# Performance work log

Hardware: AMD Instinct MI355X
Metric: run time of the kernel (lower is better)

## Reference

```python
import jax, jax.numpy as jnp
import numpy as np

EPS = 1e-07

def setup_inputs() -> dict:
    key = jax.random.key(0)
    kx, kw, kb, ku = jax.random.split(key, 4)
    B, S, D, A = 1024, 512, 200, 100
    x = jax.random.normal(kx, (B, S, D), dtype=jnp.float32)
    W = jax.random.normal(kw, (D, A), dtype=jnp.float32)
    b = jax.random.normal(kb, (A,), dtype=jnp.float32)
    u = jax.random.normal(ku, (A, 1), dtype=jnp.float32)
    return {"x": x, "W": W, "b": b, "u": u}

def reference(x, W, b, u):
    # uit: [B,S,A] = tanh(x @ W + b)
    uit = jnp.tanh(jnp.einsum('bsd,da->bsa', x, W) + b)
    # ait: [B,S] raw scores -> exp -> normalize over seq (faithful: no max-subtract)
    ait = jnp.exp(jnp.einsum('bsa,a->bs', uit, u[:, 0]))
    ait = ait / (jnp.sum(ait, axis=1, keepdims=True) + EPS)
    # weighted sum pool over seq: [B,D]
    return jnp.einsum('bsd,bs->bd', x, ait)
```

## Files before the change

### kernel.cpp

```cpp
#include <hip/hip_runtime.h>
#include <math.h>


typedef _Float16 half8 __attribute__((ext_vector_type(8)));
typedef float float4_ __attribute__((ext_vector_type(4)));

#define B_   1024
#define S_   512
#define D_   200
#define A_   100
#define NPAD 128
#define KPAD 224
#define SC   64
#define PITCH 228

#define WT_BYTES (NPAD * KPAD * 2)

__global__ void prep_kernel(const float* __restrict__ W,
                            const float* __restrict__ bias,
                            const float* __restrict__ u,
                            void* __restrict__ ws) {
  _Float16* wt = (_Float16*)ws;
  float* upad = (float*)((char*)ws + WT_BYTES);
  float* bpad = upad + NPAD;
  int idx = blockIdx.x * 256 + threadIdx.x;
  if (idx < NPAD * KPAD) {
    int n = idx / KPAD;
    int k = idx % KPAD;
    float v = (n < A_ && k < D_) ? W[k * A_ + n] : 0.f;
    wt[idx] = (_Float16)v;
  }
  if (blockIdx.x == 0 && threadIdx.x < NPAD) {
    int t = threadIdx.x;
    upad[t] = (t < A_) ? u[t] : 0.f;
    bpad[t] = (t < A_) ? bias[t] : 0.f;
  }
}

__global__ __launch_bounds__(256, 2)
void attn_kernel(const float* __restrict__ x,
                 const void* __restrict__ ws,
                 float* __restrict__ out) {
  __shared__ float xs[SC * PITCH];
  __shared__ float score_part[4][SC];
  __shared__ float e_lds[SC];

  const int b    = blockIdx.x;
  const int tid  = threadIdx.x;
  const int lane = tid & 63;
  const int wave = tid >> 6;
  const int lm   = lane & 15;
  const int lq   = lane >> 4;

  const _Float16* wt = (const _Float16*)ws;
  const float* upad = (const float*)((const char*)ws + WT_BYTES);
  const float* bpad = upad + NPAD;

  half8 Bfrag[2][7];
  float ureg[2], breg[2];
#pragma unroll
  for (int nn = 0; nn < 2; ++nn) {
    int a = (2 * wave + nn) * 16 + lm;
#pragma unroll
    for (int k = 0; k < 7; ++k) {
      Bfrag[nn][k] = *(const half8*)(wt + (size_t)a * KPAD + k * 32 + lq * 8);
    }
    ureg[nn] = upad[a];
    breg[nn] = bpad[a];
  }

  float acc_out = 0.f, den = 0.f;

  for (int chunk = 0; chunk < S_ / SC; ++chunk) {
    __syncthreads();

    {
      int c  = tid & 63;
      int r0 = tid >> 6;
      const float* xg = x + ((size_t)b * S_ + (size_t)chunk * SC) * D_;
#pragma unroll
      for (int j = 0; j < 16; ++j) {
        int row = r0 + 4 * j;
        if (c < 50) {
          float4_ v = *(const float4_*)(xg + row * D_ + c * 4);
          *(float4_*)(&xs[row * PITCH + c * 4]) = v;
        } else if (c < 57) {
          float4_ z = {0.f, 0.f, 0.f, 0.f};
          *(float4_*)(&xs[row * PITCH + c * 4]) = z;
        }
      }
    }
    __syncthreads();

    float4_ acc[4][2];
#pragma unroll
    for (int m = 0; m < 4; ++m)
#pragma unroll
      for (int nn = 0; nn < 2; ++nn)
        acc[m][nn] = (float4_){0.f, 0.f, 0.f, 0.f};

#pragma unroll
    for (int k = 0; k < 7; ++k) {
      half8 af[4];
#pragma unroll
      for (int m = 0; m < 4; ++m) {
        int row = m * 16 + lm;
        int col = k * 32 + lq * 8;
        float4_ lo = *(const float4_*)(&xs[row * PITCH + col]);
        float4_ hi = *(const float4_*)(&xs[row * PITCH + col + 4]);
        half8 a;
        a[0] = (_Float16)lo.x; a[1] = (_Float16)lo.y;
        a[2] = (_Float16)lo.z; a[3] = (_Float16)lo.w;
        a[4] = (_Float16)hi.x; a[5] = (_Float16)hi.y;
        a[6] = (_Float16)hi.z; a[7] = (_Float16)hi.w;
        af[m] = a;
      }
#pragma unroll
      for (int m = 0; m < 4; ++m)
#pragma unroll
        for (int nn = 0; nn < 2; ++nn)
          acc[m][nn] = __builtin_amdgcn_mfma_f32_16x16x32_f16(
              af[m], Bfrag[nn][k], acc[m][nn], 0, 0, 0);
    }

    float p[4][4];
#pragma unroll
    for (int m = 0; m < 4; ++m) {
#pragma unroll
      for (int r = 0; r < 4; ++r) {
        float s0 = 0.f;
#pragma unroll
        for (int nn = 0; nn < 2; ++nn) {
          float z  = acc[m][nn][r] + breg[nn];
          float az = fabsf(z);
          float ez = __expf(az + az);
          float rc = __builtin_amdgcn_rcpf(ez + 1.f);
          float t  = fmaf(-2.f, rc, 1.f);
          t = copysignf(t, z);
          s0 = fmaf(t, ureg[nn], s0);
        }
        p[m][r] = s0;
      }
    }
#pragma unroll
    for (int m = 0; m < 4; ++m) {
#pragma unroll
      for (int r = 0; r < 4; ++r) {
        float v = p[m][r];
        v += __shfl_xor(v, 1);
        v += __shfl_xor(v, 2);
        v += __shfl_xor(v, 4);
        v += __shfl_xor(v, 8);
        p[m][r] = v;
      }
    }
    if (lm == 0) {
#pragma unroll
      for (int m = 0; m < 4; ++m)
#pragma unroll
        for (int r = 0; r < 4; ++r)
          score_part[wave][m * 16 + lq * 4 + r] = p[m][r];
    }
    __syncthreads();

    if (tid < SC) {
      float ssum = score_part[0][tid] + score_part[1][tid] +
                   score_part[2][tid] + score_part[3][tid];
      e_lds[tid] = __expf(ssum);
    }
    __syncthreads();

    if (tid < D_) {
#pragma unroll 4
      for (int s = 0; s < SC; ++s) {
        float e = e_lds[s];
        den += e;
        acc_out = fmaf(e, xs[s * PITCH + tid], acc_out);
      }
    }
  }

  if (tid < D_) {
    out[(size_t)b * D_ + tid] = acc_out / (den + 1e-7f);
  }
}

extern "C" void kernel_launch(void* const* d_in, const int* in_sizes, int n_in,
                              void* d_out, int out_size, void* d_ws, size_t ws_size,
                              hipStream_t stream) {
  const float* x = (const float*)d_in[0];
  const float* W = (const float*)d_in[1];
  const float* b = (const float*)d_in[2];
  const float* u = (const float*)d_in[3];
  float* out = (float*)d_out;

  int prep_elems = NPAD * KPAD;
  int prep_blocks = (prep_elems + 255) / 256;
  prep_kernel<<<prep_blocks, 256, 0, stream>>>(W, b, u, d_ws);

  attn_kernel<<<B_, 256, 0, stream>>>(x, d_ws, out);
}
```

Before: 651.1 us.

## Split sequence chunks across blocks with fp16 LDS tile and separate reduction kernel

Each batch row's eight sequence chunks now run as independent blocks, each writing partial numerator and denominator sums to workspace. A new reduce kernel combines them and normalizes. The x tile is converted to fp16 once when stored in LDS, which halves LDS use and allows higher occupancy (launch bounds raised to 4 blocks per CU). The aim is to replace the serial per-block chunk loop with far more parallel memory traffic. The cost is an extra kernel launch and partial-sum traffic, and the pooling sum now uses fp16-rounded x.

Measured after the change: 589.6 us. -9.5%, faster.

```diff
diff --git a/kernel.cpp b/kernel.cpp
--- a/kernel.cpp
+++ b/kernel.cpp
@@ -3,6 +3,7 @@
 
 
 typedef _Float16 half8 __attribute__((ext_vector_type(8)));
+typedef _Float16 half4_ __attribute__((ext_vector_type(4)));
 typedef float float4_ __attribute__((ext_vector_type(4)));
 
 #define B_   1024
@@ -12,9 +13,13 @@
 #define NPAD 128
 #define KPAD 224
 #define SC   64
-#define PITCH 228
+#define NCH  (S_ / SC)
+#define PITCH_H 232
 
 #define WT_BYTES (NPAD * KPAD * 2)
+#define UB_BYTES (NPAD * 2 * 4)
+#define NUM_OFF  (WT_BYTES + UB_BYTES)
+#define DEN_OFF  (NUM_OFF + (size_t)B_ * NCH * D_ * 4)
 
 __global__ void prep_kernel(const float* __restrict__ W,
                             const float* __restrict__ bias,
@@ -37,15 +42,16 @@
   }
 }
 
-__global__ __launch_bounds__(256, 2)
+__global__ __launch_bounds__(256, 4)
 void attn_kernel(const float* __restrict__ x,
-                 const void* __restrict__ ws,
-                 float* __restrict__ out) {
-  __shared__ float xs[SC * PITCH];
+                 void* __restrict__ ws) {
+  __shared__ _Float16 xs[SC * PITCH_H];
   __shared__ float score_part[4][SC];
   __shared__ float e_lds[SC];
 
-  const int b    = blockIdx.x;
+  const int blk  = blockIdx.x;
+  const int b    = blk >> 3;
+  const int chunk= blk & 7;
   const int tid  = threadIdx.x;
   const int lane = tid & 63;
   const int wave = tid >> 6;
@@ -55,6 +61,8 @@
   const _Float16* wt = (const _Float16*)ws;
   const float* upad = (const float*)((const char*)ws + WT_BYTES);
   const float* bpad = upad + NPAD;
+  float* num_out = (float*)((char*)ws + NUM_OFF);
+  float* den_out = (float*)((char*)ws + DEN_OFF);
 
   half8 Bfrag[2][7];
   float ureg[2], breg[2];
@@ -62,126 +70,124 @@
   for (int nn = 0; nn < 2; ++nn) {
     int a = (2 * wave + nn) * 16 + lm;
 #pragma unroll
-    for (int k = 0; k < 7; ++k) {
+    for (int k = 0; k < 7; ++k)
       Bfrag[nn][k] = *(const half8*)(wt + (size_t)a * KPAD + k * 32 + lq * 8);
-    }
     ureg[nn] = upad[a];
     breg[nn] = bpad[a];
   }
 
-  float acc_out = 0.f, den = 0.f;
-
-  for (int chunk = 0; chunk < S_ / SC; ++chunk) {
-    __syncthreads();
-
-    {
-      int c  = tid & 63;
-      int r0 = tid >> 6;
-      const float* xg = x + ((size_t)b * S_ + (size_t)chunk * SC) * D_;
-#pragma unroll
-      for (int j = 0; j < 16; ++j) {
-        int row = r0 + 4 * j;
-        if (c < 50) {
-          float4_ v = *(const float4_*)(xg + row * D_ + c * 4);
-          *(float4_*)(&xs[row * PITCH + c * 4]) = v;
-        } else if (c < 57) {
-          float4_ z = {0.f, 0.f, 0.f, 0.f};
-          *(float4_*)(&xs[row * PITCH + c * 4]) = z;
-        }
+  {
+    int c  = tid & 63;
+    int r0 = tid >> 6;
+    const float* xg = x + ((size_t)b * S_ + (size_t)chunk * SC) * D_;
+#pragma unroll
+    for (int j = 0; j < 16; ++j) {
+      int row = r0 + 4 * j;
+      if (c < 50) {
+        float4_ v = *(const float4_*)(xg + row * D_ + c * 4);
+        half4_ h = {(_Float16)v.x, (_Float16)v.y, (_Float16)v.z, (_Float16)v.w};
+        *(half4_*)(&xs[row * PITCH_H + c * 4]) = h;
+      } else if (c < 56) {
+        half4_ z = {(_Float16)0.f, (_Float16)0.f, (_Float16)0.f, (_Float16)0.f};
+        *(half4_*)(&xs[row * PITCH_H + c * 4]) = z;
       }
     }
-    __syncthreads();
-
-    float4_ acc[4][2];
+  }
+  __syncthreads();
+
+  float4_ acc[4][2];
+#pragma unroll
+  for (int m = 0; m < 4; ++m)
+#pragma unroll
+    for (int nn = 0; nn < 2; ++nn)
+      acc[m][nn] = (float4_){0.f, 0.f, 0.f, 0.f};
+
+#pragma unroll
+  for (int k = 0; k < 7; ++k) {
+    half8 af[4];
 #pragma unroll
     for (int m = 0; m < 4; ++m)
+      af[m] = *(const half8*)(&xs[(m * 16 + lm) * PITCH_H + k * 32 + lq * 8]);
+#pragma unroll
+    for (int m = 0; m < 4; ++m)
 #pragma unroll
       for (int nn = 0; nn < 2; ++nn)
-        acc[m][nn] = (float4_){0.f, 0.f, 0.f, 0.f};
-
-#pragma unroll
-    for (int k = 0; k < 7; ++k) {
-      half8 af[4];
-#pragma unroll
-      for (int m = 0; m < 4; ++m) {
-        int row = m * 16 + lm;
-        int col = k * 32 + lq * 8;
-        float4_ lo = *(const float4_*)(&xs[row * PITCH + col]);
-        float4_ hi = *(const float4_*)(&xs[row * PITCH + col + 4]);
-        half8 a;
-        a[0] = (_Float16)lo.x; a[1] = (_Float16)lo.y;
-        a[2] = (_Float16)lo.z; a[3] = (_Float16)lo.w;
-        a[4] = (_Float16)hi.x; a[5] = (_Float16)hi.y;
-        a[6] = (_Float16)hi.z; a[7] = (_Float16)hi.w;
-        af[m] = a;
+        acc[m][nn] = __builtin_amdgcn_mfma_f32_16x16x32_f16(
+            af[m], Bfrag[nn][k], acc[m][nn], 0, 0, 0);
+  }
+
+  float p[4][4];
+#pragma unroll
+  for (int m = 0; m < 4; ++m) {
+#pragma unroll
+    for (int r = 0; r < 4; ++r) {
+      float s0 = 0.f;
+#pragma unroll
+      for (int nn = 0; nn < 2; ++nn) {
+        float z  = acc[m][nn][r] + breg[nn];
+        float az = fabsf(z);
+        float ez = __expf(az + az);
+        float rc = __builtin_amdgcn_rcpf(ez + 1.f);
+        float t  = fmaf(-2.f, rc, 1.f);
+        t = copysignf(t, z);
+        s0 = fmaf(t, ureg[nn], s0);
       }
-#pragma unroll
-      for (int m = 0; m < 4; ++m)
-#pragma unroll
-        for (int nn = 0; nn < 2; ++nn)
-          acc[m][nn] = __builtin_amdgcn_mfma_f32_16x16x32_f16(
-              af[m], Bfrag[nn][k], acc[m][nn], 0, 0, 0);
+      float v = s0;
+      v += __shfl_xor(v, 1);
+      v += __shfl_xor(v, 2);
+      v += __shfl_xor(v, 4);
+      v += __shfl_xor(v, 8);
+      p[m][r] = v;
     }
-
-    float p[4][4];
-#pragma unroll
-    for (int m = 0; m < 4; ++m) {
-#pragma unroll
-      for (int r = 0; r < 4; ++r) {
-        float s0 = 0.f;
-#pragma unroll
-        for (int nn = 0; nn < 2; ++nn) {
-          float z  = acc[m][nn][r] + breg[nn];
-          float az = fabsf(z);
-          float ez = __expf(az + az);
-          float rc = __builtin_amdgcn_rcpf(ez + 1.f);
-          float t  = fmaf(-2.f, rc, 1.f);
-          t = copysignf(t, z);
-          s0 = fmaf(t, ureg[nn], s0);
-        }
-        p[m][r] = s0;
-      }
+  }
+  if (lm == 0) {
+#pragma unroll
+    for (int m = 0; m < 4; ++m)
+#pragma unroll
+      for (int r = 0; r < 4; ++r)
+        score_part[wave][m * 16 + lq * 4 + r] = p[m][r];
+  }
+  __syncthreads();
+
+  if (tid < SC) {
+    float ssum = score_part[0][tid] + score_part[1][tid] +
+                 score_part[2][tid] + score_part[3][tid];
+    float e = __expf(ssum);
+    e_lds[tid] = e;
+    float d = e;
+    d += __shfl_xor(d, 1);
+    d += __shfl_xor(d, 2);
+    d += __shfl_xor(d, 4);
+    d += __shfl_xor(d, 8);
+    d += __shfl_xor(d, 16);
+    d += __shfl_xor(d, 32);
+    if (tid == 0) den_out[blk] = d;
+  }
+  __syncthreads();
+
+  if (tid < D_) {
+    float accv = 0.f;
+#pragma unroll 4
+    for (int s = 0; s < SC; ++s)
+      accv = fmaf(e_lds[s], (float)xs[s * PITCH_H + tid], accv);
+    num_out[(size_t)blk * D_ + tid] = accv;
+  }
+}
+
+__global__ __launch_bounds__(256)
+void reduce_kernel(const void* __restrict__ ws, float* __restrict__ out) {
+  const float* num = (const float*)((const char*)ws + NUM_OFF);
+  const float* den = (const float*)((const char*)ws + DEN_OFF);
+  int b = blockIdx.x;
+  int tid = threadIdx.x;
+  if (tid < D_) {
+    float s = 0.f, d = 0.f;
+#pragma unroll
+    for (int c = 0; c < NCH; ++c) {
+      s += num[(size_t)(b * NCH + c) * D_ + tid];
+      d += den[b * NCH + c];
     }
-#pragma unroll
-    for (int m = 0; m < 4; ++m) {
-#pragma unroll
-      for (int r = 0; r < 4; ++r) {
-        float v = p[m][r];
-        v += __shfl_xor(v, 1);
-        v += __shfl_xor(v, 2);
-        v += __shfl_xor(v, 4);
-        v += __shfl_xor(v, 8);
-        p[m][r] = v;
-      }
-    }
-    if (lm == 0) {
-#pragma unroll
-      for (int m = 0; m < 4; ++m)
-#pragma unroll
-        for (int r = 0; r < 4; ++r)
-          score_part[wave][m * 16 + lq * 4 + r] = p[m][r];
-    }
-    __syncthreads();
-
-    if (tid < SC) {
-      float ssum = score_part[0][tid] + score_part[1][tid] +
-                   score_part[2][tid] + score_part[3][tid];
-      e_lds[tid] = __expf(ssum);
-    }
-    __syncthreads();
-
-    if (tid < D_) {
-#pragma unroll 4
-      for (int s = 0; s < SC; ++s) {
-        float e = e_lds[s];
-        den += e;
-        acc_out = fmaf(e, xs[s * PITCH + tid], acc_out);
-      }
-    }
-  }
-
-  if (tid < D_) {
-    out[(size_t)b * D_ + tid] = acc_out / (den + 1e-7f);
+    out[(size_t)b * D_ + tid] = s / (d + 1e-7f);
   }
 }
 
@@ -197,6 +203,6 @@
   int prep_elems = NPAD * KPAD;
   int prep_blocks = (prep_elems + 255) / 256;
   prep_kernel<<<prep_blocks, 256, 0, stream>>>(W, b, u, d_ws);
-
-  attn_kernel<<<B_, 256, 0, stream>>>(x, d_ws, out);
-}
+  attn_kernel<<<B_ * NCH, 256, 0, stream>>>(x, d_ws);
+  reduce_kernel<<<B_, 256, 0, stream>>>(d_ws, out);
+}
```
